# Performance work log

Measured on AMD Instinct MI355X. Metric: run time of the kernel, lower is better.

Reference implementation:

```python
import jax, jax.numpy as jnp
import numpy as np

N_NODES = 51200
N_GRAPHS = 64
NODES_PER_GRAPH = 800
N_EDGES = 819200
DIM_IN = 128
DIM_HIDDEN = 64
HEADS = 3
DIM_OUT = 64


def leaky(x, slope):
    return jnp.where(x >= 0, x, slope * x)


def setup_inputs() -> dict:
    key = jax.random.key(0)
    ks = jax.random.split(key, 12)
    s = lambda fan_in: 1.0 / np.sqrt(fan_in)
    X = jax.random.normal(ks[0], (N_NODES, DIM_IN), dtype=jnp.float32)
    edge_indices = jax.random.randint(ks[1], (2, N_EDGES), 0, N_NODES, dtype=jnp.int32)
    ptr = (jnp.arange(N_GRAPHS + 1, dtype=jnp.int32) * NODES_PER_GRAPH)
    # linearSeq: Linear(dim_in, dim_hidden) + LeakyReLU
    W1 = jax.random.uniform(ks[2], (DIM_IN, DIM_HIDDEN), jnp.float32, -s(DIM_IN), s(DIM_IN))
    b1 = jax.random.uniform(ks[3], (DIM_HIDDEN,), jnp.float32, -s(DIM_IN), s(DIM_IN))
    # GATConv params: lin_src/lin_dst (no bias), att_src/att_dst, bias (concat=False -> out_channels)
    W_src = jax.random.uniform(ks[4], (DIM_HIDDEN, HEADS * DIM_HIDDEN), jnp.float32, -s(DIM_HIDDEN), s(DIM_HIDDEN))
    W_dst = jax.random.uniform(ks[5], (DIM_HIDDEN, HEADS * DIM_HIDDEN), jnp.float32, -s(DIM_HIDDEN), s(DIM_HIDDEN))
    att_src = jax.random.normal(ks[6], (HEADS, DIM_HIDDEN), dtype=jnp.float32) * 0.1
    att_dst = jax.random.normal(ks[7], (HEADS, DIM_HIDDEN), dtype=jnp.float32) * 0.1
    gat_bias = jnp.zeros((DIM_HIDDEN,), dtype=jnp.float32)
    # linear_final: Linear(2*dim_hidden, dim_out)
    Wf = jax.random.uniform(ks[8], (2 * DIM_HIDDEN, DIM_OUT), jnp.float32, -s(2 * DIM_HIDDEN), s(2 * DIM_HIDDEN))
    bf = jax.random.uniform(ks[9], (DIM_OUT,), jnp.float32, -s(2 * DIM_HIDDEN), s(2 * DIM_HIDDEN))
    return {"X": X, "W1": W1, "b1": b1, "W_src": W_src, "W_dst": W_dst,
            "att_src": att_src, "att_dst": att_dst, "gat_bias": gat_bias,
            "Wf": Wf, "bf": bf, "edge_indices": edge_indices, "ptr": ptr}


def reference(X, W1, b1, W_src, W_dst, att_src, att_dst, gat_bias, Wf, bf, edge_indices, ptr):
    N = X.shape[0]
    src, dst = edge_indices[0], edge_indices[1]  # message flows src -> dst
    # input projection
    h = leaky(X @ W1 + b1, 0.01)                                  # [N, DH]
    # GATConv (heads=3, concat=False, add_self_loops=False)
    x_src = (h @ W_src).reshape(N, HEADS, DIM_HIDDEN)             # [N, H, C]
    x_dst = (h @ W_dst).reshape(N, HEADS, DIM_HIDDEN)
    a_src = jnp.einsum('nhc,hc->nh', x_src, att_src)              # [N, H]
    a_dst = jnp.einsum('nhc,hc->nh', x_dst, att_dst)
    logits = leaky(a_src[src] + a_dst[dst], 0.2)                  # [E, H]
    # segment softmax over incoming edges of each target node
    m = jax.ops.segment_max(logits, dst, num_segments=N)          # [N, H]
    e = jnp.exp(logits - m[dst])
    denom = jax.ops.segment_sum(e, dst, num_segments=N)           # [N, H]
    attn = e / denom[dst]                                         # [E, H]
    msg = x_src[src] * attn[..., None]                            # [E, H, C]
    agg = jax.ops.segment_sum(msg, dst, num_segments=N)           # [N, H, C]
    out = agg.mean(axis=1) + gat_bias                             # concat=False -> head mean
    # final head
    cat = jnp.concatenate([h, out], axis=1)                       # [N, 2*DH]
    y = leaky(cat, 0.01) @ Wf + bf                                # [N, DO]
    # aggregate_using_ptr: mean-pool nodes per graph using CSR ptr
    node_graph = jnp.searchsorted(ptr, jnp.arange(N), side='right') - 1
    sums = jax.ops.segment_sum(y, node_graph, num_segments=ptr.shape[0] - 1)
    counts = (ptr[1:] - ptr[:-1]).astype(y.dtype)
    pooled = sums / counts[:, None]                               # [n_graphs, DO]
    return pooled, attn
```

## Files before the change

kernel.cpp:

```cpp
#include <hip/hip_runtime.h>
#include <hip/hip_bf16.h>

#define N_NODES   51200
#define N_GRAPHS  64
#define N_EDGES   819200
#define DIM_IN    128
#define DH        64
#define HEADS     3
#define DIM_OUT   64
#define CAP       96
#define NPART     8
#define PART_SZ   (N_NODES / NPART)
#define PBUF_CAP  131072
#define BIN_BLOCKS  (N_EDGES / 2048)
#define PREP_BLOCKS 116
#define SC2_BLOCKS  (NPART * (PBUF_CAP / 2048))
#define K1_BLOCKS   (N_NODES / 64)

typedef __hip_bfloat16 bf16;
typedef short bf16x8 __attribute__((ext_vector_type(8)));
typedef float f32x4  __attribute__((ext_vector_type(4)));

__device__ __forceinline__ float b2f(bf16 x) { return __bfloat162float(x); }
__device__ __forceinline__ bf16  f2b(float x) { return __float2bfloat16(x); }
__device__ __forceinline__ short f2bs(float x) { return (short)__bfloat16_as_ushort(f2b(x)); }
__device__ __forceinline__ float leaky(float x, float s) { return x >= 0.f ? x : s * x; }
__device__ __forceinline__ float ldin(const void* p, size_t i, int f32) {
    return f32 ? ((const float*)p)[i] : b2f(((const bf16*)p)[i]);
}
__device__ __forceinline__ bf16x8 ld8(const void* p, size_t i, int f32) {
    if (!f32) return *((const bf16x8*)((const short*)p + i));
    const float* f = (const float*)p + i;
    bf16x8 r;
    #pragma unroll
    for (int j = 0; j < 8; ++j) r[j] = f2bs(f[j]);
    return r;
}

__global__ __launch_bounds__(256) void detect_kernel(const unsigned short* __restrict__ Xu,
                                                     int* __restrict__ flag) {
    __shared__ int cnt;
    int tid = threadIdx.x;
    if (tid == 0) cnt = 0;
    __syncthreads();
    int local = 0;
    for (int i = tid * 2; i < 8192; i += 512) {
        unsigned e = (Xu[i] >> 7) & 0xFF;
        if (e >= 110 && e <= 135) local++;
    }
    atomicAdd(&cnt, local);
    __syncthreads();
    if (tid == 0) *flag = (cnt < 2048) ? 1 : 0;
}

__global__ __launch_bounds__(256) void k_bin_prep(const int* __restrict__ src,
                                                  const int* __restrict__ dst,
                                                  int* __restrict__ pcur,
                                                  unsigned* __restrict__ pbuf,
                                                  const void* __restrict__ W1,
                                                  const void* __restrict__ Wsrc,
                                                  const void* __restrict__ Wdst,
                                                  const void* __restrict__ Wf,
                                                  const void* __restrict__ att_src,
                                                  const void* __restrict__ att_dst,
                                                  const int* __restrict__ flagp,
                                                  short* __restrict__ W1t,
                                                  short* __restrict__ Wspt,
                                                  short* __restrict__ Wft,
                                                  short* __restrict__ Wat) {
    if (blockIdx.x < BIN_BLOCKS) {
        __shared__ int cnt[NPART];
        __shared__ int base[NPART];
        const int tid = threadIdx.x;
        if (tid < NPART) cnt[tid] = 0;
        __syncthreads();
        const int e0 = blockIdx.x * 2048;
        unsigned pk[8]; int pp[8]; int rr[8];
        #pragma unroll
        for (int t = 0; t < 8; ++t) {
            int e = e0 + t * 256 + tid;
            int s = src[e], d = dst[e];
            int p = d / PART_SZ;
            pk[t] = ((unsigned)s << 16) | (unsigned)d;
            pp[t] = p;
            rr[t] = atomicAdd(&cnt[p], 1);
        }
        __syncthreads();
        if (tid < NPART) base[tid] = atomicAdd(&pcur[tid], cnt[tid]);
        __syncthreads();
        #pragma unroll
        for (int t = 0; t < 8; ++t) {
            int p = pp[t];
            int o = base[p] + rr[t];
            if (o < PBUF_CAP) pbuf[(size_t)p * PBUF_CAP + o] = pk[t];
        }
        return;
    }
    const int f32 = *flagp;
    int idx = (blockIdx.x - BIN_BLOCKS) * 256 + threadIdx.x;
    if (idx < 8192) {
        int n = idx >> 7, k = idx & 127;
        W1t[idx] = f2bs(ldin(W1, (size_t)k * 64 + n, f32));
    } else if (idx < 20480) {
        int j = idx - 8192;
        int col = j / 192;
        int rem = j - col * 192;
        int hh = rem >> 6, kk = rem & 63;
        Wspt[j] = f2bs(ldin(Wsrc, (size_t)kk * 192 + hh * 64 + col, f32) * (1.0f / 3.0f));
    } else if (idx < 28672) {
        int j = idx - 20480;
        int n = j >> 7, k = j & 127;
        Wft[j] = f2bs(ldin(Wf, (size_t)k * 64 + n, f32));
    } else if (idx < 29696) {
        int j = idx - 28672;
        int n = j >> 6, k = j & 63;
        float v = 0.f;
        if (n < 3) {
            for (int c = 0; c < 64; ++c)
                v += ldin(Wsrc, (size_t)k * 192 + n * 64 + c, f32) * ldin(att_src, n * 64 + c, f32);
        } else if (n < 6) {
            for (int c = 0; c < 64; ++c)
                v += ldin(Wdst, (size_t)k * 192 + (n - 3) * 64 + c, f32) * ldin(att_dst, (n - 3) * 64 + c, f32);
        }
        Wat[j] = f2bs(v);
    }
}

__global__ __launch_bounds__(256) void k_scatter_k1(const unsigned* __restrict__ pbuf,
                                                    const int* __restrict__ pcur,
                                                    int* __restrict__ cursor,
                                                    unsigned short* __restrict__ bucket,
                                                    const void* __restrict__ X,
                                                    const short* __restrict__ W1t,
                                                    const short* __restrict__ Wat,
                                                    const void* __restrict__ b1,
                                                    const int* __restrict__ flagp,
                                                    bf16* __restrict__ h_bf,
                                                    unsigned char* __restrict__ h8,
                                                    float* __restrict__ a_src4,
                                                    float* __restrict__ a_dst4) {
    if (blockIdx.x < SC2_BLOCKS) {
        const int p = blockIdx.x & (NPART - 1);
        const int slice = blockIdx.x >> 3;
        const int pc = min(pcur[p], PBUF_CAP);
        const unsigned* pb = pbuf + (size_t)p * PBUF_CAP;
        const int base = slice * 2048 + threadIdx.x;
        #pragma unroll
        for (int t = 0; t < 8; ++t) {
            int i = base + t * 256;
            if (i < pc) {
                unsigned pk = pb[i];
                int d = (int)(pk & 0xFFFFu);
                int pos = atomicAdd(&cursor[d], 1);
                if (pos < CAP) bucket[(size_t)d * CAP + pos] = (unsigned short)(pk >> 16);
            }
        }
        return;
    }
    const int f32 = *flagp;
    __shared__ short hs[64 * 72];
    const int tid  = threadIdx.x;
    const int w    = tid >> 6;
    const int lane = tid & 63;
    const int lm   = lane & 15;
    const int q    = lane >> 4;
    const int row0 = (blockIdx.x - SC2_BLOCKS) * 64;

    const float bias = ldin(b1, w * 16 + lm, f32);
    for (int mt = 0; mt < 4; ++mt) {
        f32x4 acc = {0.f, 0.f, 0.f, 0.f};
        #pragma unroll
        for (int kc = 0; kc < 4; ++kc) {
            bf16x8 a = ld8(X, (size_t)(row0 + mt * 16 + lm) * 128 + kc * 32 + q * 8, f32);
            bf16x8 b = *((const bf16x8*)(W1t + (size_t)(w * 16 + lm) * 128 + kc * 32 + q * 8));
            acc = __builtin_amdgcn_mfma_f32_16x16x32_bf16(a, b, acc, 0, 0, 0);
        }
        #pragma unroll
        for (int r = 0; r < 4; ++r) {
            int row = mt * 16 + q * 4 + r;
            float v = leaky(acc[r] + bias, 0.01f);
            short hv = f2bs(v);
            hs[row * 72 + w * 16 + lm] = hv;
            h_bf[(size_t)(row0 + row) * 64 + w * 16 + lm] = __ushort_as_bfloat16((unsigned short)hv);
            h8[(size_t)(row0 + row) * 64 + w * 16 + lm] =
                (unsigned char)__builtin_amdgcn_cvt_pk_fp8_f32(v, 0.f, 0, false);
        }
    }
    __syncthreads();

    {
        const int mt = w;
        bf16x8 a0  = *((const bf16x8*)(hs + (mt * 16 + lm) * 72 + q * 8));
        bf16x8 a1  = *((const bf16x8*)(hs + (mt * 16 + lm) * 72 + 32 + q * 8));
        bf16x8 b0  = *((const bf16x8*)(Wat + (size_t)lm * 64 + q * 8));
        bf16x8 b1v = *((const bf16x8*)(Wat + (size_t)lm * 64 + 32 + q * 8));
        f32x4 acca = {0.f, 0.f, 0.f, 0.f};
        acca = __builtin_amdgcn_mfma_f32_16x16x32_bf16(a0, b0, acca, 0, 0, 0);
        acca = __builtin_amdgcn_mfma_f32_16x16x32_bf16(a1, b1v, acca, 0, 0, 0);
        if (lm < 6) {
            #pragma unroll
            for (int r = 0; r < 4; ++r) {
                int row = row0 + mt * 16 + q * 4 + r;
                if (lm < 3) a_src4[(size_t)row * 4 + lm] = acca[r];
                else        a_dst4[(size_t)row * 4 + (lm - 3)] = acca[r];
            }
        }
    }
}

__global__ __launch_bounds__(256) void edge_kernel(const unsigned short* __restrict__ bucket,
                                                   const int* __restrict__ cursor,
                                                   const float* __restrict__ a_src4,
                                                   const float* __restrict__ a_dst4,
                                                   const unsigned char* __restrict__ h8,
                                                   float4* __restrict__ dstinfo,
                                                   bf16* __restrict__ wagg) {
    const int lane = threadIdx.x & 63;
    const int w = threadIdx.x >> 6;
    const int n = blockIdx.x * 4 + w;
    const int dg = min(cursor[n], CAP);
    const float4 ad = ((const float4*)a_dst4)[n];
    __shared__ float4 buf[4][64];
    float den0 = 0.f, den1 = 0.f, den2 = 0.f;
    float acc0 = 0.f, acc1 = 0.f, acc2 = 0.f;
    for (int c0 = 0; c0 < dg; c0 += 64) {
        int cnt = min(64, dg - c0);
        if (lane < cnt) {
            int s = bucket[n * CAP + c0 + lane];
            const float4 as = ((const float4*)a_src4)[s];
            float e0 = __expf(leaky(as.x + ad.x, 0.2f));
            float e1 = __expf(leaky(as.y + ad.y, 0.2f));
            float e2 = __expf(leaky(as.z + ad.z, 0.2f));
            den0 += e0; den1 += e1; den2 += e2;
            buf[w][lane] = make_float4(e0, e1, e2, __int_as_float(s));
        }
        asm volatile("s_waitcnt lgkmcnt(0)" ::: "memory");
        int j = 0;
        for (; j + 8 <= cnt; j += 8) {
            float4 r[8]; int hv[8];
            #pragma unroll
            for (int u = 0; u < 8; ++u) r[u] = buf[w][j + u];
            #pragma unroll
            for (int u = 0; u < 8; ++u)
                hv[u] = (int)h8[(((unsigned)__float_as_int(r[u].w)) << 6) | (unsigned)lane];
            #pragma unroll
            for (int u = 0; u < 8; ++u) {
                float f = __builtin_amdgcn_cvt_f32_fp8(hv[u], 0);
                acc0 += r[u].x * f; acc1 += r[u].y * f; acc2 += r[u].z * f;
            }
        }
        for (; j < cnt; ++j) {
            float4 r = buf[w][j];
            int hvv = (int)h8[(((unsigned)__float_as_int(r.w)) << 6) | (unsigned)lane];
            float f = __builtin_amdgcn_cvt_f32_fp8(hvv, 0);
            acc0 += r.x * f; acc1 += r.y * f; acc2 += r.z * f;
        }
    }
    #pragma unroll
    for (int off = 32; off >= 1; off >>= 1) {
        den0 += __shfl_xor(den0, off);
        den1 += __shfl_xor(den1, off);
        den2 += __shfl_xor(den2, off);
    }
    float inv0 = den0 > 0.f ? 1.f / den0 : 0.f;
    float inv1 = den1 > 0.f ? 1.f / den1 : 0.f;
    float inv2 = den2 > 0.f ? 1.f / den2 : 0.f;
    size_t wb = (size_t)n * 192;
    wagg[wb + lane]       = f2b(acc0 * inv0);
    wagg[wb + 64 + lane]  = f2b(acc1 * inv1);
    wagg[wb + 128 + lane] = f2b(acc2 * inv2);
    if (lane == 0) {
        dstinfo[(size_t)n * 2 + 0] = make_float4(ad.x, ad.y, ad.z, 0.f);
        dstinfo[(size_t)n * 2 + 1] = make_float4(inv0, inv1, inv2, 0.f);
    }
}

__global__ __launch_bounds__(256) void attn_g3_kernel(const int* __restrict__ src,
                                                      const int* __restrict__ dst,
                                                      const float* __restrict__ a_src4,
                                                      const float4* __restrict__ dstinfo,
                                                      const bf16* __restrict__ h_bf,
                                                      const bf16* __restrict__ wagg,
                                                      const short* __restrict__ Wspt,
                                                      const short* __restrict__ Wft,
                                                      const void* __restrict__ gat_bias,
                                                      const void* __restrict__ bfv,
                                                      const int* __restrict__ flagp,
                                                      bf16* __restrict__ y_bf,
                                                      void* __restrict__ d_out) {
    const int f32 = *flagp;
    __shared__ short cs[64 * 136];
    if (blockIdx.x < N_EDGES / 256) {
        int e = blockIdx.x * 256 + threadIdx.x;
        int s = src[e], d = dst[e];
        const float4 as = ((const float4*)a_src4)[s];
        const float4 ad = dstinfo[(size_t)d * 2 + 0];
        const float4 cv = dstinfo[(size_t)d * 2 + 1];
        float a0 = __expf(leaky(as.x + ad.x, 0.2f)) * cv.x;
        float a1 = __expf(leaky(as.y + ad.y, 0.2f)) * cv.y;
        float a2 = __expf(leaky(as.z + ad.z, 0.2f)) * cv.z;
        size_t o = (size_t)N_GRAPHS * DIM_OUT + (size_t)e * 3;
        if (f32) {
            float* p = (float*)d_out;
            p[o] = a0; p[o + 1] = a1; p[o + 2] = a2;
        } else {
            bf16* p = (bf16*)d_out;
            p[o] = f2b(a0); p[o + 1] = f2b(a1); p[o + 2] = f2b(a2);
        }
        return;
    }
    const int bid  = blockIdx.x - N_EDGES / 256;
    const int tid  = threadIdx.x;
    const int w    = tid >> 6;
    const int lane = tid & 63;
    const int lm   = lane & 15;
    const int q    = lane >> 4;
    const int row0 = bid * 64;
    for (int idx = tid; idx < 64 * 64; idx += 256) {
        int r = idx >> 6, k = idx & 63;
        cs[r * 136 + k] = f2bs(leaky(b2f(h_bf[(size_t)(row0 + r) * 64 + k]), 0.01f));
    }
    {
        const int col = w * 16 + lm;
        const float gb = ldin(gat_bias, col, f32);
        for (int mt = 0; mt < 4; ++mt) {
            f32x4 acc = {0.f, 0.f, 0.f, 0.f};
            #pragma unroll
            for (int kc = 0; kc < 6; ++kc) {
                bf16x8 a = *((const bf16x8*)((const short*)wagg + (size_t)(row0 + mt * 16 + lm) * 192 + kc * 32 + q * 8));
                bf16x8 b = *((const bf16x8*)(Wspt + (size_t)col * 192 + kc * 32 + q * 8));
                acc = __builtin_amdgcn_mfma_f32_16x16x32_bf16(a, b, acc, 0, 0, 0);
            }
            #pragma unroll
            for (int r = 0; r < 4; ++r) {
                int row = mt * 16 + q * 4 + r;
                cs[row * 136 + 64 + col] = f2bs(leaky(acc[r] + gb, 0.01f));
            }
        }
    }
    __syncthreads();
    const float bias = ldin(bfv, w * 16 + lm, f32);
    for (int mt = 0; mt < 4; ++mt) {
        f32x4 acc = {0.f, 0.f, 0.f, 0.f};
        #pragma unroll
        for (int kc = 0; kc < 4; ++kc) {
            bf16x8 a = *((const bf16x8*)(cs + (mt * 16 + lm) * 136 + kc * 32 + q * 8));
            bf16x8 b = *((const bf16x8*)(Wft + (size_t)(w * 16 + lm) * 128 + kc * 32 + q * 8));
            acc = __builtin_amdgcn_mfma_f32_16x16x32_bf16(a, b, acc, 0, 0, 0);
        }
        #pragma unroll
        for (int r = 0; r < 4; ++r) {
            int row = row0 + mt * 16 + q * 4 + r;
            y_bf[(size_t)row * 64 + w * 16 + lm] = f2b(acc[r] + bias);
        }
    }
}

__global__ __launch_bounds__(1024) void pool_kernel(const bf16* __restrict__ y_bf,
                                                    const int* __restrict__ ptr,
                                                    const int* __restrict__ flagp,
                                                    void* __restrict__ d_out) {
    __shared__ float part[16][64];
    const int f32 = *flagp;
    const int g = blockIdx.x;
    const int w = threadIdx.x >> 6, lane = threadIdx.x & 63;
    const int lo = ptr[g], hi = ptr[g + 1];
    const int cnt = hi - lo;
    float s = 0.f;
    for (int i = lo + w; i < hi; i += 16) s += b2f(y_bf[(size_t)i * DIM_OUT + lane]);
    part[w][lane] = s;
    __syncthreads();
    if (threadIdx.x < 64) {
        float t = 0.f;
        #pragma unroll
        for (int k = 0; k < 16; ++k) t += part[k][threadIdx.x];
        float v = t / (float)cnt;
        if (f32) ((float*)d_out)[g * DIM_OUT + threadIdx.x] = v;
        else     ((bf16*)d_out)[g * DIM_OUT + threadIdx.x]  = f2b(v);
    }
}

extern "C" void kernel_launch(void* const* d_in, const int* in_sizes, int n_in,
                              void* d_out, int out_size, void* d_ws, size_t ws_size,
                              hipStream_t stream) {
    const void* X        = d_in[0];
    const void* W1       = d_in[1];
    const void* b1       = d_in[2];
    const void* Wsrc     = d_in[3];
    const void* Wdst     = d_in[4];
    const void* att_src  = d_in[5];
    const void* att_dst  = d_in[6];
    const void* gat_bias = d_in[7];
    const void* Wf       = d_in[8];
    const void* bfv      = d_in[9];
    const int*  ei       = (const int*)d_in[10];
    const int*  ptr      = (const int*)d_in[11];
    const int*  src  = ei;
    const int*  dstp = ei + N_EDGES;

    char* ws = (char*)d_ws;
    size_t off_b = 0;
    auto alloc = [&](size_t bytes) -> char* {
        char* p = ws + off_b;
        off_b += (bytes + 255) & ~(size_t)255;
        return p;
    };
    int*     flag    = (int*)    alloc(256);
    short*   W1t     = (short*)  alloc(8192 * 2);
    short*   Wspt    = (short*)  alloc(12288 * 2);
    short*   Wft     = (short*)  alloc(8192 * 2);
    short*   Wat     = (short*)  alloc(1024 * 2);
    bf16*    h_bf    = (bf16*)   alloc((size_t)N_NODES * 64 * 2);
    unsigned char* h8 = (unsigned char*)alloc((size_t)N_NODES * 64);
    float*   a_src4  = (float*)  alloc((size_t)N_NODES * 16);
    float*   a_dst4  = (float*)  alloc((size_t)N_NODES * 16);
    float4*  dstinfo = (float4*) alloc((size_t)N_NODES * 2 * 16);
    bf16*    wagg    = (bf16*)   alloc((size_t)N_NODES * 192 * 2);
    int*     pcur    = (int*)    alloc(256);
    int*     cursor  = (int*)    alloc((size_t)N_NODES * 4);
    unsigned short* bucket = (unsigned short*)alloc((size_t)N_NODES * CAP * 2);
    unsigned* pbuf   = (unsigned*)wagg;
    bf16*    y_bf    = (bf16*)   bucket;
    if (off_b > ws_size) return;

    hipLaunchKernelGGL(detect_kernel, dim3(1), dim3(256), 0, stream,
                       (const unsigned short*)X, flag);
    hipMemsetAsync(pcur, 0, 256 + (size_t)N_NODES * 4, stream);
    hipLaunchKernelGGL(k_bin_prep, dim3(BIN_BLOCKS + PREP_BLOCKS), dim3(256), 0, stream,
                       src, dstp, pcur, pbuf,
                       W1, Wsrc, Wdst, Wf, att_src, att_dst, flag, W1t, Wspt, Wft, Wat);
    hipLaunchKernelGGL(k_scatter_k1, dim3(SC2_BLOCKS + K1_BLOCKS), dim3(256), 0, stream,
                       pbuf, pcur, cursor, bucket,
                       X, W1t, Wat, b1, flag, h_bf, h8, a_src4, a_dst4);
    hipLaunchKernelGGL(edge_kernel, dim3(N_NODES / 4), dim3(256), 0, stream,
                       bucket, cursor, a_src4, a_dst4, h8, dstinfo, wagg);
    hipLaunchKernelGGL(attn_g3_kernel, dim3(N_EDGES / 256 + N_NODES / 64), dim3(256), 0, stream,
                       src, dstp, a_src4, dstinfo, h_bf, wagg, Wspt, Wft,
                       gat_bias, bfv, flag, y_bf, d_out);
    hipLaunchKernelGGL(pool_kernel, dim3(N_GRAPHS), dim3(1024), 0, stream, y_bf, ptr, flag, d_out);
}
```

Before: 237.1 us.

## Fuse all pipeline stages into one persistent cooperative kernel with grid syncs

Replaces the six separate launches (detect, bin/prep, scatter/k1, edge, attn/g3, pool) with one persistent cooperative kernel. Its blocks loop over virtual block indices and separate the phases with grid.sync(). The aim is to remove per-launch overhead and the gaps between dependent kernels. In exchange the grid is capped by occupancy (at most 1024 blocks), grid-wide barriers cost something, and register pressure from the merged code may lower per-phase throughput. The prep blocks now recompute the f32/bf16 detection locally on a smaller sample instead of reading the flag, which can disagree with the flag used elsewhere.

```diff
diff --git a/kernel.cpp b/kernel.cpp
--- a/kernel.cpp
+++ b/kernel.cpp
@@ -1,5 +1,8 @@
 #include <hip/hip_runtime.h>
 #include <hip/hip_bf16.h>
+#include <hip/hip_cooperative_groups.h>
+
+namespace cg = cooperative_groups;
 
 #define N_NODES   51200
 #define N_GRAPHS  64
@@ -12,10 +15,18 @@
 #define NPART     8
 #define PART_SZ   (N_NODES / NPART)
 #define PBUF_CAP  131072
-#define BIN_BLOCKS  (N_EDGES / 2048)
-#define PREP_BLOCKS 116
-#define SC2_BLOCKS  (NPART * (PBUF_CAP / 2048))
-#define K1_BLOCKS   (N_NODES / 64)
+
+#define GRID_BLKS 1024
+#define PH0_BIN   (N_EDGES / 2048)
+#define PH0_PREP  116
+#define PH0_TOT   (PH0_BIN + PH0_PREP + 1)
+#define PH1_SC    (NPART * (PBUF_CAP / 2048))
+#define PH1_K1    (N_NODES / 64)
+#define PH1_TOT   (PH1_SC + PH1_K1)
+#define PH2_TOT   (N_NODES / 4)
+#define PH3_ATT   (N_EDGES / 256)
+#define PH3_G3    (N_NODES / 64)
+#define PH3_TOT   (PH3_ATT + PH3_G3)
 
 typedef __hip_bfloat16 bf16;
 typedef short bf16x8 __attribute__((ext_vector_type(8)));
@@ -37,366 +48,317 @@
     return r;
 }
 
-__global__ __launch_bounds__(256) void detect_kernel(const unsigned short* __restrict__ Xu,
-                                                     int* __restrict__ flag) {
-    __shared__ int cnt;
-    int tid = threadIdx.x;
-    if (tid == 0) cnt = 0;
-    __syncthreads();
-    int local = 0;
-    for (int i = tid * 2; i < 8192; i += 512) {
-        unsigned e = (Xu[i] >> 7) & 0xFF;
-        if (e >= 110 && e <= 135) local++;
-    }
-    atomicAdd(&cnt, local);
-    __syncthreads();
-    if (tid == 0) *flag = (cnt < 2048) ? 1 : 0;
-}
-
-__global__ __launch_bounds__(256) void k_bin_prep(const int* __restrict__ src,
-                                                  const int* __restrict__ dst,
-                                                  int* __restrict__ pcur,
-                                                  unsigned* __restrict__ pbuf,
-                                                  const void* __restrict__ W1,
-                                                  const void* __restrict__ Wsrc,
-                                                  const void* __restrict__ Wdst,
-                                                  const void* __restrict__ Wf,
-                                                  const void* __restrict__ att_src,
-                                                  const void* __restrict__ att_dst,
-                                                  const int* __restrict__ flagp,
-                                                  short* __restrict__ W1t,
-                                                  short* __restrict__ Wspt,
-                                                  short* __restrict__ Wft,
-                                                  short* __restrict__ Wat) {
-    if (blockIdx.x < BIN_BLOCKS) {
-        __shared__ int cnt[NPART];
-        __shared__ int base[NPART];
-        const int tid = threadIdx.x;
-        if (tid < NPART) cnt[tid] = 0;
+struct GParams {
+    const int* src; const int* dst; const int* ptr;
+    const void *X, *W1, *b1, *Wsrc, *Wdst, *att_src, *att_dst, *gat_bias, *Wf, *bfv;
+    int* flag; int* pcur; unsigned* pbuf; int* cursor; unsigned short* bucket;
+    short *W1t, *Wspt, *Wft, *Wat;
+    bf16* h_bf; unsigned char* h8; float* a_src4; float* a_dst4;
+    float4* dstinfo; bf16* wagg; bf16* y_bf; void* d_out;
+};
+
+__global__ __launch_bounds__(256, 4) void giga_kernel(GParams P) {
+    cg::grid_group grid = cg::this_grid();
+    __shared__ __align__(16) char smem[64 * 136 * 2];
+    const int tid = threadIdx.x;
+
+    for (int vb = blockIdx.x; vb < PH0_TOT; vb += gridDim.x) {
+        if (vb < PH0_BIN) {
+            int* cnt  = (int*)smem;
+            int* base = cnt + NPART;
+            if (tid < NPART) cnt[tid] = 0;
+            __syncthreads();
+            const int e0 = vb * 2048;
+            unsigned pk[8]; int pp[8]; int rr[8];
+            #pragma unroll
+            for (int t = 0; t < 8; ++t) {
+                int e = e0 + t * 256 + tid;
+                int s = P.src[e], d = P.dst[e];
+                int p = d / PART_SZ;
+                pk[t] = ((unsigned)s << 16) | (unsigned)d;
+                pp[t] = p;
+                rr[t] = atomicAdd(&cnt[p], 1);
+            }
+            __syncthreads();
+            if (tid < NPART) base[tid] = atomicAdd(&P.pcur[tid], cnt[tid]);
+            __syncthreads();
+            #pragma unroll
+            for (int t = 0; t < 8; ++t) {
+                int o = base[pp[t]] + rr[t];
+                if (o < PBUF_CAP) P.pbuf[(size_t)pp[t] * PBUF_CAP + o] = pk[t];
+            }
+            __syncthreads();
+        } else if (vb < PH0_BIN + PH0_PREP) {
+            unsigned ex = (((const unsigned short*)P.X)[2 * tid] >> 7) & 0xFF;
+            int c = __syncthreads_count(ex >= 110 && ex <= 135);
+            const int bf32 = (c < 128) ? 1 : 0;
+            int idx = (vb - PH0_BIN) * 256 + tid;
+            if (idx < 8192) {
+                int n = idx >> 7, k = idx & 127;
+                P.W1t[idx] = f2bs(ldin(P.W1, (size_t)k * 64 + n, bf32));
+            } else if (idx < 20480) {
+                int j = idx - 8192;
+                int col = j / 192;
+                int rem = j - col * 192;
+                int hh = rem >> 6, kk = rem & 63;
+                P.Wspt[j] = f2bs(ldin(P.Wsrc, (size_t)kk * 192 + hh * 64 + col, bf32) * (1.0f / 3.0f));
+            } else if (idx < 28672) {
+                int j = idx - 20480;
+                int n = j >> 7, k = j & 127;
+                P.Wft[j] = f2bs(ldin(P.Wf, (size_t)k * 64 + n, bf32));
+            } else if (idx < 29696) {
+                int j = idx - 28672;
+                int n = j >> 6, k = j & 63;
+                float v = 0.f;
+                if (n < 3) {
+                    for (int c2 = 0; c2 < 64; ++c2)
+                        v += ldin(P.Wsrc, (size_t)k * 192 + n * 64 + c2, bf32) * ldin(P.att_src, n * 64 + c2, bf32);
+                } else if (n < 6) {
+                    for (int c2 = 0; c2 < 64; ++c2)
+                        v += ldin(P.Wdst, (size_t)k * 192 + (n - 3) * 64 + c2, bf32) * ldin(P.att_dst, (n - 3) * 64 + c2, bf32);
+                }
+                P.Wat[j] = f2bs(v);
+            }
+            __syncthreads();
+        } else {
+            int* cntp = (int*)smem;
+            if (tid == 0) *cntp = 0;
+            __syncthreads();
+            int local = 0;
+            const unsigned short* Xu = (const unsigned short*)P.X;
+            for (int i = tid * 2; i < 8192; i += 512) {
+                unsigned e = (Xu[i] >> 7) & 0xFF;
+                if (e >= 110 && e <= 135) local++;
+            }
+            atomicAdd(cntp, local);
+            __syncthreads();
+            if (tid == 0) *P.flag = (*cntp < 2048) ? 1 : 0;
+            __syncthreads();
+        }
+    }
+    grid.sync();
+    const int f32 = *P.flag;
+
+    for (int vb = blockIdx.x; vb < PH1_TOT; vb += gridDim.x) {
+        if (vb < PH1_SC) {
+            const int p = vb & (NPART - 1);
+            const int slice = vb >> 3;
+            const int pc = min(P.pcur[p], PBUF_CAP);
+            const unsigned* pb = P.pbuf + (size_t)p * PBUF_CAP;
+            const int base = slice * 2048 + tid;
+            #pragma unroll
+            for (int t = 0; t < 8; ++t) {
+                int i = base + t * 256;
+                if (i < pc) {
+                    unsigned pk = pb[i];
+                    int d = (int)(pk & 0xFFFFu);
+                    int pos = atomicAdd(&P.cursor[d], 1);
+                    if (pos < CAP) P.bucket[(size_t)d * CAP + pos] = (unsigned short)(pk >> 16);
+                }
+            }
+        } else {
+            short* hs = (short*)smem;
+            const int w    = tid >> 6;
+            const int lane = tid & 63;
+            const int lm   = lane & 15;
+            const int q    = lane >> 4;
+            const int row0 = (vb - PH1_SC) * 64;
+            const float bias = ldin(P.b1, w * 16 + lm, f32);
+            for (int mt = 0; mt < 4; ++mt) {
+                f32x4 acc = {0.f, 0.f, 0.f, 0.f};
+                #pragma unroll
+                for (int kc = 0; kc < 4; ++kc) {
+                    bf16x8 a = ld8(P.X, (size_t)(row0 + mt * 16 + lm) * 128 + kc * 32 + q * 8, f32);
+                    bf16x8 b = *((const bf16x8*)(P.W1t + (size_t)(w * 16 + lm) * 128 + kc * 32 + q * 8));
+                    acc = __builtin_amdgcn_mfma_f32_16x16x32_bf16(a, b, acc, 0, 0, 0);
+                }
+                #pragma unroll
+                for (int r = 0; r < 4; ++r) {
+                    int row = mt * 16 + q * 4 + r;
+                    float v = leaky(acc[r] + bias, 0.01f);
+                    short hv = f2bs(v);
+                    hs[row * 72 + w * 16 + lm] = hv;
+                    P.h_bf[(size_t)(row0 + row) * 64 + w * 16 + lm] = __ushort_as_bfloat16((unsigned short)hv);
+                    P.h8[(size_t)(row0 + row) * 64 + w * 16 + lm] =
+                        (unsigned char)__builtin_amdgcn_cvt_pk_fp8_f32(v, 0.f, 0, false);
+                }
+            }
+            __syncthreads();
+            {
+                const int mt = w;
+                bf16x8 a0  = *((const bf16x8*)(hs + (mt * 16 + lm) * 72 + q * 8));
+                bf16x8 a1  = *((const bf16x8*)(hs + (mt * 16 + lm) * 72 + 32 + q * 8));
+                bf16x8 b0  = *((const bf16x8*)(P.Wat + (size_t)lm * 64 + q * 8));
+                bf16x8 b1v = *((const bf16x8*)(P.Wat + (size_t)lm * 64 + 32 + q * 8));
+                f32x4 acca = {0.f, 0.f, 0.f, 0.f};
+                acca = __builtin_amdgcn_mfma_f32_16x16x32_bf16(a0, b0, acca, 0, 0, 0);
+                acca = __builtin_amdgcn_mfma_f32_16x16x32_bf16(a1, b1v, acca, 0, 0, 0);
+                if (lm < 6) {
+                    #pragma unroll
+                    for (int r = 0; r < 4; ++r) {
+                        int row = row0 + mt * 16 + q * 4 + r;
+                        if (lm < 3) P.a_src4[(size_t)row * 4 + lm] = acca[r];
+                        else        P.a_dst4[(size_t)row * 4 + (lm - 3)] = acca[r];
+                    }
+                }
+            }
+            __syncthreads();
+        }
+    }
+    grid.sync();
+
+    for (int vb = blockIdx.x; vb < PH2_TOT; vb += gridDim.x) {
+        const int lane = tid & 63;
+        const int w = tid >> 6;
+        const int n = vb * 4 + w;
+        const int dg = min(P.cursor[n], CAP);
+        const float4 ad = ((const float4*)P.a_dst4)[n];
+        float4* buf = ((float4*)smem) + w * 64;
+        float den0 = 0.f, den1 = 0.f, den2 = 0.f;
+        float acc0 = 0.f, acc1 = 0.f, acc2 = 0.f;
+        for (int c0 = 0; c0 < dg; c0 += 64) {
+            int cnt = min(64, dg - c0);
+            if (lane < cnt) {
+                int s = P.bucket[(size_t)n * CAP + c0 + lane];
+                const float4 as = ((const float4*)P.a_src4)[s];
+                float e0 = __expf(leaky(as.x + ad.x, 0.2f));
+                float e1 = __expf(leaky(as.y + ad.y, 0.2f));
+                float e2 = __expf(leaky(as.z + ad.z, 0.2f));
+                den0 += e0; den1 += e1; den2 += e2;
+                buf[lane] = make_float4(e0, e1, e2, __int_as_float(s));
+            }
+            asm volatile("s_waitcnt lgkmcnt(0)" ::: "memory");
+            int j = 0;
+            for (; j + 8 <= cnt; j += 8) {
+                float4 r[8]; int hv[8];
+                #pragma unroll
+                for (int u = 0; u < 8; ++u) r[u] = buf[j + u];
+                #pragma unroll
+                for (int u = 0; u < 8; ++u)
+                    hv[u] = (int)P.h8[(((unsigned)__float_as_int(r[u].w)) << 6) | (unsigned)lane];
+                #pragma unroll
+                for (int u = 0; u < 8; ++u) {
+                    float f = __builtin_amdgcn_cvt_f32_fp8(hv[u], 0);
+                    acc0 += r[u].x * f; acc1 += r[u].y * f; acc2 += r[u].z * f;
+                }
+            }
+            for (; j < cnt; ++j) {
+                float4 r = buf[j];
+                int hvv = (int)P.h8[(((unsigned)__float_as_int(r.w)) << 6) | (unsigned)lane];
+                float f = __builtin_amdgcn_cvt_f32_fp8(hvv, 0);
+                acc0 += r.x * f; acc1 += r.y * f; acc2 += r.z * f;
+            }
+        }
+        #pragma unroll
+        for (int off = 32; off >= 1; off >>= 1) {
+            den0 += __shfl_xor(den0, off);
+            den1 += __shfl_xor(den1, off);
+            den2 += __shfl_xor(den2, off);
+        }
+        float inv0 = den0 > 0.f ? 1.f / den0 : 0.f;
+        float inv1 = den1 > 0.f ? 1.f / den1 : 0.f;
+        float inv2 = den2 > 0.f ? 1.f / den2 : 0.f;
+        size_t wb = (size_t)n * 192;
+        P.wagg[wb + lane]       = f2b(acc0 * inv0);
+        P.wagg[wb + 64 + lane]  = f2b(acc1 * inv1);
+        P.wagg[wb + 128 + lane] = f2b(acc2 * inv2);
+        if (lane == 0) {
+            P.dstinfo[(size_t)n * 2 + 0] = make_float4(ad.x, ad.y, ad.z, 0.f);
+            P.dstinfo[(size_t)n * 2 + 1] = make_float4(inv0, inv1, inv2, 0.f);
+        }
+    }
+    grid.sync();
+
+    for (int vb = blockIdx.x; vb < PH3_TOT; vb += gridDim.x) {
+        if (vb < PH3_ATT) {
+            int e = vb * 256 + tid;
+            int s = P.src[e], d = P.dst[e];
+            const float4 as = ((const float4*)P.a_src4)[s];
+            const float4 ad = P.dstinfo[(size_t)d * 2 + 0];
+            const float4 cv = P.dstinfo[(size_t)d * 2 + 1];
+            float a0 = __expf(leaky(as.x + ad.x, 0.2f)) * cv.x;
+            float a1 = __expf(leaky(as.y + ad.y, 0.2f)) * cv.y;
+            float a2 = __expf(leaky(as.z + ad.z, 0.2f)) * cv.z;
+            size_t o = (size_t)N_GRAPHS * DIM_OUT + (size_t)e * 3;
+            if (f32) {
+                float* p = (float*)P.d_out;
+                p[o] = a0; p[o + 1] = a1; p[o + 2] = a2;
+            } else {
+                bf16* p = (bf16*)P.d_out;
+                p[o] = f2b(a0); p[o + 1] = f2b(a1); p[o + 2] = f2b(a2);
+            }
+        } else {
+            short* cs = (short*)smem;
+            const int w    = tid >> 6;
+            const int lane = tid & 63;
+            const int lm   = lane & 15;
+            const int q    = lane >> 4;
+            const int row0 = (vb - PH3_ATT) * 64;
+            for (int idx = tid; idx < 64 * 64; idx += 256) {
+                int r = idx >> 6, k = idx & 63;
+                cs[r * 136 + k] = f2bs(leaky(b2f(P.h_bf[(size_t)(row0 + r) * 64 + k]), 0.01f));
+            }
+            {
+                const int col = w * 16 + lm;
+                const float gb = ldin(P.gat_bias, col, f32);
+                for (int mt = 0; mt < 4; ++mt) {
+                    f32x4 acc = {0.f, 0.f, 0.f, 0.f};
+                    #pragma unroll
+                    for (int kc = 0; kc < 6; ++kc) {
+                        bf16x8 a = *((const bf16x8*)((const short*)P.wagg + (size_t)(row0 + mt * 16 + lm) * 192 + kc * 32 + q * 8));
+                        bf16x8 b = *((const bf16x8*)(P.Wspt + (size_t)col * 192 + kc * 32 + q * 8));
+                        acc = __builtin_amdgcn_mfma_f32_16x16x32_bf16(a, b, acc, 0, 0, 0);
+                    }
+                    #pragma unroll
+                    for (int r = 0; r < 4; ++r) {
+                        int row = mt * 16 + q * 4 + r;
+                        cs[row * 136 + 64 + col] = f2bs(leaky(acc[r] + gb, 0.01f));
+                    }
+                }
+            }
+            __syncthreads();
+            const float bias = ldin(P.bfv, w * 16 + lm, f32);
+            for (int mt = 0; mt < 4; ++mt) {
+                f32x4 acc = {0.f, 0.f, 0.f, 0.f};
+                #pragma unroll
+                for (int kc = 0; kc < 4; ++kc) {
+                    bf16x8 a = *((const bf16x8*)(cs + (mt * 16 + lm) * 136 + kc * 32 + q * 8));
+                    bf16x8 b = *((const bf16x8*)(P.Wft + (size_t)(w * 16 + lm) * 128 + kc * 32 + q * 8));
+                    acc = __builtin_amdgcn_mfma_f32_16x16x32_bf16(a, b, acc, 0, 0, 0);
+                }
+                #pragma unroll
+                for (int r = 0; r < 4; ++r) {
+                    int row = row0 + mt * 16 + q * 4 + r;
+                    P.y_bf[(size_t)row * 64 + w * 16 + lm] = f2b(acc[r] + bias);
+                }
+            }
+            __syncthreads();
+        }
+    }
+    grid.sync();
+
+    for (int vb = blockIdx.x; vb < N_GRAPHS; vb += gridDim.x) {
+        float* part = (float*)smem;
+        const int w = tid >> 6, lane = tid & 63;
+        const int lo = P.ptr[vb], hi = P.ptr[vb + 1];
+        float s = 0.f;
+        for (int i = lo + w; i < hi; i += 4) s += b2f(P.y_bf[(size_t)i * DIM_OUT + lane]);
+        part[w * 64 + lane] = s;
         __syncthreads();
-        const int e0 = blockIdx.x * 2048;
-        unsigned pk[8]; int pp[8]; int rr[8];
-        #pragma unroll
-        for (int t = 0; t < 8; ++t) {
-            int e = e0 + t * 256 + tid;
-            int s = src[e], d = dst[e];
-            int p = d / PART_SZ;
-            pk[t] = ((unsigned)s << 16) | (unsigned)d;
-            pp[t] = p;
-            rr[t] = atomicAdd(&cnt[p], 1);
+        if (tid < 64) {
+            float t4 = part[tid] + part[64 + tid] + part[128 + tid] + part[192 + tid];
+            float v = t4 / (float)(hi - lo);
+            if (f32) ((float*)P.d_out)[vb * DIM_OUT + tid] = v;
+            else     ((bf16*)P.d_out)[vb * DIM_OUT + tid]  = f2b(v);
         }
         __syncthreads();
-        if (tid < NPART) base[tid] = atomicAdd(&pcur[tid], cnt[tid]);
-        __syncthreads();
-        #pragma unroll
-        for (int t = 0; t < 8; ++t) {
-            int p = pp[t];
-            int o = base[p] + rr[t];
-            if (o < PBUF_CAP) pbuf[(size_t)p * PBUF_CAP + o] = pk[t];
-        }
-        return;
-    }
-    const int f32 = *flagp;
-    int idx = (blockIdx.x - BIN_BLOCKS) * 256 + threadIdx.x;
-    if (idx < 8192) {
-        int n = idx >> 7, k = idx & 127;
-        W1t[idx] = f2bs(ldin(W1, (size_t)k * 64 + n, f32));
-    } else if (idx < 20480) {
-        int j = idx - 8192;
-        int col = j / 192;
-        int rem = j - col * 192;
-        int hh = rem >> 6, kk = rem & 63;
-        Wspt[j] = f2bs(ldin(Wsrc, (size_t)kk * 192 + hh * 64 + col, f32) * (1.0f / 3.0f));
-    } else if (idx < 28672) {
-        int j = idx - 20480;
-        int n = j >> 7, k = j & 127;
-        Wft[j] = f2bs(ldin(Wf, (size_t)k * 64 + n, f32));
-    } else if (idx < 29696) {
-        int j = idx - 28672;
-        int n = j >> 6, k = j & 63;
-        float v = 0.f;
-        if (n < 3) {
-            for (int c = 0; c < 64; ++c)
-                v += ldin(Wsrc, (size_t)k * 192 + n * 64 + c, f32) * ldin(att_src, n * 64 + c, f32);
-        } else if (n < 6) {
-            for (int c = 0; c < 64; ++c)
-                v += ldin(Wdst, (size_t)k * 192 + (n - 3) * 64 + c, f32) * ldin(att_dst, (n - 3) * 64 + c, f32);
-        }
-        Wat[j] = f2bs(v);
-    }
-}
-
-__global__ __launch_bounds__(256) void k_scatter_k1(const unsigned* __restrict__ pbuf,
-                                                    const int* __restrict__ pcur,
-                                                    int* __restrict__ cursor,
-                                                    unsigned short* __restrict__ bucket,
-                                                    const void* __restrict__ X,
-                                                    const short* __restrict__ W1t,
-                                                    const short* __restrict__ Wat,
-                                                    const void* __restrict__ b1,
-                                                    const int* __restrict__ flagp,
-                                                    bf16* __restrict__ h_bf,
-                                                    unsigned char* __restrict__ h8,
-                                                    float* __restrict__ a_src4,
-                                                    float* __restrict__ a_dst4) {
-    if (blockIdx.x < SC2_BLOCKS) {
-        const int p = blockIdx.x & (NPART - 1);
-        const int slice = blockIdx.x >> 3;
-        const int pc = min(pcur[p], PBUF_CAP);
-        const unsigned* pb = pbuf + (size_t)p * PBUF_CAP;
-        const int base = slice * 2048 + threadIdx.x;
-        #pragma unroll
-        for (int t = 0; t < 8; ++t) {
-            int i = base + t * 256;
-            if (i < pc) {
-                unsigned pk = pb[i];
-                int d = (int)(pk & 0xFFFFu);
-                int pos = atomicAdd(&cursor[d], 1);
-                if (pos < CAP) bucket[(size_t)d * CAP + pos] = (unsigned short)(pk >> 16);
-            }
-        }
-        return;
-    }
-    const int f32 = *flagp;
-    __shared__ short hs[64 * 72];
-    const int tid  = threadIdx.x;
-    const int w    = tid >> 6;
-    const int lane = tid & 63;
-    const int lm   = lane & 15;
-    const int q    = lane >> 4;
-    const int row0 = (blockIdx.x - SC2_BLOCKS) * 64;
-
-    const float bias = ldin(b1, w * 16 + lm, f32);
-    for (int mt = 0; mt < 4; ++mt) {
-        f32x4 acc = {0.f, 0.f, 0.f, 0.f};
-        #pragma unroll
-        for (int kc = 0; kc < 4; ++kc) {
-            bf16x8 a = ld8(X, (size_t)(row0 + mt * 16 + lm) * 128 + kc * 32 + q * 8, f32);
-            bf16x8 b = *((const bf16x8*)(W1t + (size_t)(w * 16 + lm) * 128 + kc * 32 + q * 8));
-            acc = __builtin_amdgcn_mfma_f32_16x16x32_bf16(a, b, acc, 0, 0, 0);
-        }
-        #pragma unroll
-        for (int r = 0; r < 4; ++r) {
-            int row = mt * 16 + q * 4 + r;
-            float v = leaky(acc[r] + bias, 0.01f);
-            short hv = f2bs(v);
-            hs[row * 72 + w * 16 + lm] = hv;
-            h_bf[(size_t)(row0 + row) * 64 + w * 16 + lm] = __ushort_as_bfloat16((unsigned short)hv);
-            h8[(size_t)(row0 + row) * 64 + w * 16 + lm] =
-                (unsigned char)__builtin_amdgcn_cvt_pk_fp8_f32(v, 0.f, 0, false);
-        }
-    }
-    __syncthreads();
-
-    {
-        const int mt = w;
-        bf16x8 a0  = *((const bf16x8*)(hs + (mt * 16 + lm) * 72 + q * 8));
-        bf16x8 a1  = *((const bf16x8*)(hs + (mt * 16 + lm) * 72 + 32 + q * 8));
-        bf16x8 b0  = *((const bf16x8*)(Wat + (size_t)lm * 64 + q * 8));
-        bf16x8 b1v = *((const bf16x8*)(Wat + (size_t)lm * 64 + 32 + q * 8));
-        f32x4 acca = {0.f, 0.f, 0.f, 0.f};
-        acca = __builtin_amdgcn_mfma_f32_16x16x32_bf16(a0, b0, acca, 0, 0, 0);
-        acca = __builtin_amdgcn_mfma_f32_16x16x32_bf16(a1, b1v, acca, 0, 0, 0);
-        if (lm < 6) {
-            #pragma unroll
-            for (int r = 0; r < 4; ++r) {
-                int row = row0 + mt * 16 + q * 4 + r;
-                if (lm < 3) a_src4[(size_t)row * 4 + lm] = acca[r];
-                else        a_dst4[(size_t)row * 4 + (lm - 3)] = acca[r];
-            }
-        }
-    }
-}
-
-__global__ __launch_bounds__(256) void edge_kernel(const unsigned short* __restrict__ bucket,
-                                                   const int* __restrict__ cursor,
-                                                   const float* __restrict__ a_src4,
-                                                   const float* __restrict__ a_dst4,
-                                                   const unsigned char* __restrict__ h8,
-                                                   float4* __restrict__ dstinfo,
-                                                   bf16* __restrict__ wagg) {
-    const int lane = threadIdx.x & 63;
-    const int w = threadIdx.x >> 6;
-    const int n = blockIdx.x * 4 + w;
-    const int dg = min(cursor[n], CAP);
-    const float4 ad = ((const float4*)a_dst4)[n];
-    __shared__ float4 buf[4][64];
-    float den0 = 0.f, den1 = 0.f, den2 = 0.f;
-    float acc0 = 0.f, acc1 = 0.f, acc2 = 0.f;
-    for (int c0 = 0; c0 < dg; c0 += 64) {
-        int cnt = min(64, dg - c0);
-        if (lane < cnt) {
-            int s = bucket[n * CAP + c0 + lane];
-            const float4 as = ((const float4*)a_src4)[s];
-            float e0 = __expf(leaky(as.x + ad.x, 0.2f));
-            float e1 = __expf(leaky(as.y + ad.y, 0.2f));
-            float e2 = __expf(leaky(as.z + ad.z, 0.2f));
-            den0 += e0; den1 += e1; den2 += e2;
-            buf[w][lane] = make_float4(e0, e1, e2, __int_as_float(s));
-        }
-        asm volatile("s_waitcnt lgkmcnt(0)" ::: "memory");
-        int j = 0;
-        for (; j + 8 <= cnt; j += 8) {
-            float4 r[8]; int hv[8];
-            #pragma unroll
-            for (int u = 0; u < 8; ++u) r[u] = buf[w][j + u];
-            #pragma unroll
-            for (int u = 0; u < 8; ++u)
-                hv[u] = (int)h8[(((unsigned)__float_as_int(r[u].w)) << 6) | (unsigned)lane];
-            #pragma unroll
-            for (int u = 0; u < 8; ++u) {
-                float f = __builtin_amdgcn_cvt_f32_fp8(hv[u], 0);
-                acc0 += r[u].x * f; acc1 += r[u].y * f; acc2 += r[u].z * f;
-            }
-        }
-        for (; j < cnt; ++j) {
-            float4 r = buf[w][j];
-            int hvv = (int)h8[(((unsigned)__float_as_int(r.w)) << 6) | (unsigned)lane];
-            float f = __builtin_amdgcn_cvt_f32_fp8(hvv, 0);
-            acc0 += r.x * f; acc1 += r.y * f; acc2 += r.z * f;
-        }
-    }
-    #pragma unroll
-    for (int off = 32; off >= 1; off >>= 1) {
-        den0 += __shfl_xor(den0, off);
-        den1 += __shfl_xor(den1, off);
-        den2 += __shfl_xor(den2, off);
-    }
-    float inv0 = den0 > 0.f ? 1.f / den0 : 0.f;
-    float inv1 = den1 > 0.f ? 1.f / den1 : 0.f;
-    float inv2 = den2 > 0.f ? 1.f / den2 : 0.f;
-    size_t wb = (size_t)n * 192;
-    wagg[wb + lane]       = f2b(acc0 * inv0);
-    wagg[wb + 64 + lane]  = f2b(acc1 * inv1);
-    wagg[wb + 128 + lane] = f2b(acc2 * inv2);
-    if (lane == 0) {
-        dstinfo[(size_t)n * 2 + 0] = make_float4(ad.x, ad.y, ad.z, 0.f);
-        dstinfo[(size_t)n * 2 + 1] = make_float4(inv0, inv1, inv2, 0.f);
-    }
-}
-
-__global__ __launch_bounds__(256) void attn_g3_kernel(const int* __restrict__ src,
-                                                      const int* __restrict__ dst,
-                                                      const float* __restrict__ a_src4,
-                                                      const float4* __restrict__ dstinfo,
-                                                      const bf16* __restrict__ h_bf,
-                                                      const bf16* __restrict__ wagg,
-                                                      const short* __restrict__ Wspt,
-                                                      const short* __restrict__ Wft,
-                                                      const void* __restrict__ gat_bias,
-                                                      const void* __restrict__ bfv,
-                                                      const int* __restrict__ flagp,
-                                                      bf16* __restrict__ y_bf,
-                                                      void* __restrict__ d_out) {
-    const int f32 = *flagp;
-    __shared__ short cs[64 * 136];
-    if (blockIdx.x < N_EDGES / 256) {
-        int e = blockIdx.x * 256 + threadIdx.x;
-        int s = src[e], d = dst[e];
-        const float4 as = ((const float4*)a_src4)[s];
-        const float4 ad = dstinfo[(size_t)d * 2 + 0];
-        const float4 cv = dstinfo[(size_t)d * 2 + 1];
-        float a0 = __expf(leaky(as.x + ad.x, 0.2f)) * cv.x;
-        float a1 = __expf(leaky(as.y + ad.y, 0.2f)) * cv.y;
-        float a2 = __expf(leaky(as.z + ad.z, 0.2f)) * cv.z;
-        size_t o = (size_t)N_GRAPHS * DIM_OUT + (size_t)e * 3;
-        if (f32) {
-            float* p = (float*)d_out;
-            p[o] = a0; p[o + 1] = a1; p[o + 2] = a2;
-        } else {
-            bf16* p = (bf16*)d_out;
-            p[o] = f2b(a0); p[o + 1] = f2b(a1); p[o + 2] = f2b(a2);
-        }
-        return;
-    }
-    const int bid  = blockIdx.x - N_EDGES / 256;
-    const int tid  = threadIdx.x;
-    const int w    = tid >> 6;
-    const int lane = tid & 63;
-    const int lm   = lane & 15;
-    const int q    = lane >> 4;
-    const int row0 = bid * 64;
-    for (int idx = tid; idx < 64 * 64; idx += 256) {
-        int r = idx >> 6, k = idx & 63;
-        cs[r * 136 + k] = f2bs(leaky(b2f(h_bf[(size_t)(row0 + r) * 64 + k]), 0.01f));
-    }
-    {
-        const int col = w * 16 + lm;
-        const float gb = ldin(gat_bias, col, f32);
-        for (int mt = 0; mt < 4; ++mt) {
-            f32x4 acc = {0.f, 0.f, 0.f, 0.f};
-            #pragma unroll
-            for (int kc = 0; kc < 6; ++kc) {
-                bf16x8 a = *((const bf16x8*)((const short*)wagg + (size_t)(row0 + mt * 16 + lm) * 192 + kc * 32 + q * 8));
-                bf16x8 b = *((const bf16x8*)(Wspt + (size_t)col * 192 + kc * 32 + q * 8));
-                acc = __builtin_amdgcn_mfma_f32_16x16x32_bf16(a, b, acc, 0, 0, 0);
-            }
-            #pragma unroll
-            for (int r = 0; r < 4; ++r) {
-                int row = mt * 16 + q * 4 + r;
-                cs[row * 136 + 64 + col] = f2bs(leaky(acc[r] + gb, 0.01f));
-            }
-        }
-    }
-    __syncthreads();
-    const float bias = ldin(bfv, w * 16 + lm, f32);
-    for (int mt = 0; mt < 4; ++mt) {
-        f32x4 acc = {0.f, 0.f, 0.f, 0.f};
-        #pragma unroll
-        for (int kc = 0; kc < 4; ++kc) {
-            bf16x8 a = *((const bf16x8*)(cs + (mt * 16 + lm) * 136 + kc * 32 + q * 8));
-            bf16x8 b = *((const bf16x8*)(Wft + (size_t)(w * 16 + lm) * 128 + kc * 32 + q * 8));
-            acc = __builtin_amdgcn_mfma_f32_16x16x32_bf16(a, b, acc, 0, 0, 0);
-        }
-        #pragma unroll
-        for (int r = 0; r < 4; ++r) {
-            int row = row0 + mt * 16 + q * 4 + r;
-            y_bf[(size_t)row * 64 + w * 16 + lm] = f2b(acc[r] + bias);
-        }
-    }
-}
-
-__global__ __launch_bounds__(1024) void pool_kernel(const bf16* __restrict__ y_bf,
-                                                    const int* __restrict__ ptr,
-                                                    const int* __restrict__ flagp,
-                                                    void* __restrict__ d_out) {
-    __shared__ float part[16][64];
-    const int f32 = *flagp;
-    const int g = blockIdx.x;
-    const int w = threadIdx.x >> 6, lane = threadIdx.x & 63;
-    const int lo = ptr[g], hi = ptr[g + 1];
-    const int cnt = hi - lo;
-    float s = 0.f;
-    for (int i = lo + w; i < hi; i += 16) s += b2f(y_bf[(size_t)i * DIM_OUT + lane]);
-    part[w][lane] = s;
-    __syncthreads();
-    if (threadIdx.x < 64) {
-        float t = 0.f;
-        #pragma unroll
-        for (int k = 0; k < 16; ++k) t += part[k][threadIdx.x];
-        float v = t / (float)cnt;
-        if (f32) ((float*)d_out)[g * DIM_OUT + threadIdx.x] = v;
-        else     ((bf16*)d_out)[g * DIM_OUT + threadIdx.x]  = f2b(v);
     }
 }
 
 extern "C" void kernel_launch(void* const* d_in, const int* in_sizes, int n_in,
                               void* d_out, int out_size, void* d_ws, size_t ws_size,
                               hipStream_t stream) {
-    const void* X        = d_in[0];
-    const void* W1       = d_in[1];
-    const void* b1       = d_in[2];
-    const void* Wsrc     = d_in[3];
-    const void* Wdst     = d_in[4];
-    const void* att_src  = d_in[5];
-    const void* att_dst  = d_in[6];
-    const void* gat_bias = d_in[7];
-    const void* Wf       = d_in[8];
-    const void* bfv      = d_in[9];
-    const int*  ei       = (const int*)d_in[10];
-    const int*  ptr      = (const int*)d_in[11];
-    const int*  src  = ei;
-    const int*  dstp = ei + N_EDGES;
+    const int* ei = (const int*)d_in[10];
 
     char* ws = (char*)d_ws;
     size_t off_b = 0;
@@ -423,19 +385,27 @@
     bf16*    y_bf    = (bf16*)   bucket;
     if (off_b > ws_size) return;
 
-    hipLaunchKernelGGL(detect_kernel, dim3(1), dim3(256), 0, stream,
-                       (const unsigned short*)X, flag);
+    GParams P;
+    P.src = ei; P.dst = ei + N_EDGES; P.ptr = (const int*)d_in[11];
+    P.X = d_in[0]; P.W1 = d_in[1]; P.b1 = d_in[2];
+    P.Wsrc = d_in[3]; P.Wdst = d_in[4]; P.att_src = d_in[5]; P.att_dst = d_in[6];
+    P.gat_bias = d_in[7]; P.Wf = d_in[8]; P.bfv = d_in[9];
+    P.flag = flag; P.pcur = pcur; P.pbuf = pbuf; P.cursor = cursor; P.bucket = bucket;
+    P.W1t = W1t; P.Wspt = Wspt; P.Wft = Wft; P.Wat = Wat;
+    P.h_bf = h_bf; P.h8 = h8; P.a_src4 = a_src4; P.a_dst4 = a_dst4;
+    P.dstinfo = dstinfo; P.wagg = wagg; P.y_bf = y_bf; P.d_out = d_out;
+
+    static int s_grid = 0;
+    if (s_grid == 0) {
+        int mb = 0;
+        if (hipOccupancyMaxActiveBlocksPerMultiprocessor(&mb, giga_kernel, 256, 0) != hipSuccess || mb < 1)
+            mb = 2;
+        long g = (long)mb * 256;
+        s_grid = (int)(g < GRID_BLKS ? g : GRID_BLKS);
+    }
+
     hipMemsetAsync(pcur, 0, 256 + (size_t)N_NODES * 4, stream);
-    hipLaunchKernelGGL(k_bin_prep, dim3(BIN_BLOCKS + PREP_BLOCKS), dim3(256), 0, stream,
-                       src, dstp, pcur, pbuf,
-                       W1, Wsrc, Wdst, Wf, att_src, att_dst, flag, W1t, Wspt, Wft, Wat);
-    hipLaunchKernelGGL(k_scatter_k1, dim3(SC2_BLOCKS + K1_BLOCKS), dim3(256), 0, stream,
-                       pbuf, pcur, cursor, bucket,
-                       X, W1t, Wat, b1, flag, h_bf, h8, a_src4, a_dst4);
-    hipLaunchKernelGGL(edge_kernel, dim3(N_NODES / 4), dim3(256), 0, stream,
-                       bucket, cursor, a_src4, a_dst4, h8, dstinfo, wagg);
-    hipLaunchKernelGGL(attn_g3_kernel, dim3(N_EDGES / 256 + N_NODES / 64), dim3(256), 0, stream,
-                       src, dstp, a_src4, dstinfo, h_bf, wagg, Wspt, Wft,
-                       gat_bias, bfv, flag, y_bf, d_out);
-    hipLaunchKernelGGL(pool_kernel, dim3(N_GRAPHS), dim3(1024), 0, stream, y_bf, ptr, flag, d_out);
+    void* args[] = { &P };
+    hipLaunchCooperativeKernel(reinterpret_cast<void*>(giga_kernel),
+                               dim3(s_grid), dim3(256), args, 0, stream);
 }
```

Measured after the change: 586.9 us. +147.5%, slower.
